# Kernel optimization log

Measured on AMD Instinct MI355X. Metric: run time of the kernel, lower is better.

## Reference

```python
import jax, jax.numpy as jnp
import numpy as np

S = 8192  # query length
T = 8192  # key/value length
D = 256   # head dim


def setup_inputs() -> dict:
    key = jax.random.key(0)
    kq, kk, kv = jax.random.split(key, 3)
    return {
        "query": jax.random.normal(kq, (S, D), dtype=jnp.float32),
        "key": jax.random.normal(kk, (T, D), dtype=jnp.float32),
        "value": jax.random.normal(kv, (T, D), dtype=jnp.float32),
    }


def reference(query, key, value):
    # attn_weights = Q @ K^T  (contract last dims, no batch dims)  -> [S, T]
    attn_weights = jnp.einsum("sd,td->st", query, key)
    # SoftmaxAttn: softmax over axes [ndim//2, ndim) == last axis for 2D
    attn_weights = jax.nn.softmax(attn_weights, axis=-1).astype(jnp.float32)
    # y = A @ V  -> [S, D]
    y = jnp.einsum("st,td->sd", attn_weights, value)
    return y
```

## Files before the change

kernel.cpp:

```cpp
#include <hip/hip_runtime.h>
#include <hip/hip_fp16.h>

#define S_LEN 8192
#define T_LEN 8192
#define D_DIM 256
#define QBLK 128
#define KVBLK 32
#define TSPLIT 8
#define TCHUNK (T_LEN / TSPLIT)
#define NKV (TCHUNK / KVBLK)
#define NQT (S_LEN / QBLK)
#define KTILE_BYTES 16384
#define VTILE_BYTES 16384
#define RESCALE_THR 6.0f
#define LOG2E 1.44269504f

typedef _Float16 f16x8 __attribute__((ext_vector_type(8)));
typedef float f32x4 __attribute__((ext_vector_type(4)));

struct h4 { _Float16 h[4]; };

#define GLOAD_LDS16(g, l)                                              \
    __builtin_amdgcn_global_load_lds(                                  \
        (const __attribute__((address_space(1))) void*)(g),            \
        (__attribute__((address_space(3))) void*)(l), 16, 0, 0)

#define MFMA16(a, b, c) __builtin_amdgcn_mfma_f32_16x16x32_f16(a, b, c, 0, 0, 0)

__global__ __launch_bounds__(256) void cvt_kernel(const float* __restrict__ in,
                                                  _Float16* __restrict__ out, int n4) {
    int i = blockIdx.x * 256 + threadIdx.x;
    if (i < n4) {
        float4 v = ((const float4*)in)[i];
        h4 o;
        o.h[0] = (_Float16)(v.x * LOG2E); o.h[1] = (_Float16)(v.y * LOG2E);
        o.h[2] = (_Float16)(v.z * LOG2E); o.h[3] = (_Float16)(v.w * LOG2E);
        ((h4*)out)[i] = o;
    }
}

__global__ __launch_bounds__(256) void cvt_swz_kernel(const float* __restrict__ in,
                                                      _Float16* __restrict__ img,
                                                      int nchunks) {
    int id = blockIdx.x * 256 + threadIdx.x;
    if (id >= nchunks) return;
    int row = id >> 5, ck = id & 31;
    int t = row >> 5, r = row & 31;
    float4 a = *(const float4*)(in + (size_t)row * D_DIM + ck * 8);
    float4 b = *(const float4*)(in + (size_t)row * D_DIM + ck * 8 + 4);
    f16x8 o;
    o[0] = (_Float16)a.x; o[1] = (_Float16)a.y; o[2] = (_Float16)a.z; o[3] = (_Float16)a.w;
    o[4] = (_Float16)b.x; o[5] = (_Float16)b.y; o[6] = (_Float16)b.z; o[7] = (_Float16)b.w;
    *(f16x8*)((char*)img + (size_t)t * KTILE_BYTES + r * 512 + ((ck ^ (r & 7)) << 4)) = o;
}

__global__ __launch_bounds__(256) void vt_swz_kernel(const float* __restrict__ V,
                                                     _Float16* __restrict__ Vimg) {
    __shared__ float tile[32][260];
    const int t = blockIdx.x;
#pragma unroll
    for (int i = 0; i < 8; ++i) {
        int idx = i * 256 + threadIdx.x;
        int kr = idx >> 6, c4 = idx & 63;
        float4 v = *(const float4*)(V + ((size_t)t * 32 + kr) * D_DIM + c4 * 4);
        tile[kr][c4 * 4 + 0] = v.x;
        tile[kr][c4 * 4 + 1] = v.y;
        tile[kr][c4 * 4 + 2] = v.z;
        tile[kr][c4 * 4 + 3] = v.w;
    }
    __syncthreads();
#pragma unroll
    for (int i = 0; i < 4; ++i) {
        int gid = i * 256 + threadIdx.x;
        int d = gid >> 2, gk = gid & 3;
        f16x8 o;
#pragma unroll
        for (int j = 0; j < 8; ++j)
            o[j] = (_Float16)tile[(j >> 2) * 16 + gk * 4 + (j & 3)][d];
        *(f16x8*)((char*)Vimg + (size_t)t * VTILE_BYTES + d * 64 +
                  ((gk ^ ((d >> 1) & 3)) << 4)) = o;
    }
}

__global__ __launch_bounds__(256, 2) void attn_kernel(
    const _Float16* __restrict__ Qh, const _Float16* __restrict__ Kimg,
    const _Float16* __restrict__ Vimg, _Float16* __restrict__ Opart,
    float* __restrict__ ml) {
    __shared__ __align__(16) char smem[65536];
    const int tid = threadIdx.x;
    const int wave = tid >> 6, lane = tid & 63;
    const int g = lane >> 4, c = lane & 15;
    const int qtile = blockIdx.x, split = blockIdx.y;
    const int tile0 = split * NKV;

    f16x8 qf[2][8];
    {
        const size_t qrow0 = (size_t)qtile * QBLK + wave * 32 + c;
#pragma unroll
        for (int mi = 0; mi < 2; ++mi)
#pragma unroll
            for (int ks = 0; ks < 8; ++ks)
                qf[mi][ks] =
                    *(const f16x8*)(Qh + (qrow0 + mi * 16) * D_DIM + (ks * 4 + g) * 8);
    }
    asm volatile("s_waitcnt vmcnt(0)" ::: "memory");

    f32x4 acc[2][16];
#pragma unroll
    for (int mi = 0; mi < 2; ++mi)
#pragma unroll
        for (int dt = 0; dt < 16; ++dt) acc[mi][dt] = (f32x4){0.f, 0.f, 0.f, 0.f};
    float m[2] = {-1e30f, -1e30f}, l[2] = {0.f, 0.f};

    const int othr = tid * 16;

    {
        const char* Kt = (const char*)Kimg + (size_t)tile0 * KTILE_BYTES;
        const char* Vt = (const char*)Vimg + (size_t)tile0 * VTILE_BYTES;
#pragma unroll
        for (int i = 0; i < 4; ++i) {
            GLOAD_LDS16(Kt + i * 4096 + othr, smem + i * 4096 + othr);
            GLOAD_LDS16(Vt + i * 4096 + othr, smem + 32768 + i * 4096 + othr);
        }
    }

    for (int kt = 0; kt < NKV; ++kt) {
        const int cur = kt & 1;
        if (kt + 1 < NKV) {
            const char* Kt = (const char*)Kimg + (size_t)(tile0 + kt + 1) * KTILE_BYTES;
            const char* Vt = (const char*)Vimg + (size_t)(tile0 + kt + 1) * VTILE_BYTES;
            const int nb = (cur ^ 1) * 16384;
#pragma unroll
            for (int i = 0; i < 4; ++i) {
                GLOAD_LDS16(Kt + i * 4096 + othr, smem + nb + i * 4096 + othr);
                GLOAD_LDS16(Vt + i * 4096 + othr, smem + 32768 + nb + i * 4096 + othr);
            }
            asm volatile("s_waitcnt vmcnt(8)" ::: "memory");
        } else {
            asm volatile("s_waitcnt vmcnt(0)" ::: "memory");
        }
        __builtin_amdgcn_s_barrier();

        const char* sK = smem + cur * 16384;
        const char* sV = smem + 32768 + cur * 16384;

        f32x4 st[2][2];
#pragma unroll
        for (int mi = 0; mi < 2; ++mi)
#pragma unroll
            for (int ct = 0; ct < 2; ++ct) st[mi][ct] = (f32x4){0.f, 0.f, 0.f, 0.f};
        __builtin_amdgcn_s_setprio(1);
#pragma unroll
        for (int ks = 0; ks < 8; ++ks) {
            const int ck = ((ks * 4 + g) ^ (c & 7)) << 4;
            f16x8 kf0 = *(const f16x8*)(sK + c * 512 + ck);
            f16x8 kf1 = *(const f16x8*)(sK + 8192 + c * 512 + ck);
            st[0][0] = MFMA16(kf0, qf[0][ks], st[0][0]);
            st[0][1] = MFMA16(kf1, qf[0][ks], st[0][1]);
            st[1][0] = MFMA16(kf0, qf[1][ks], st[1][0]);
            st[1][1] = MFMA16(kf1, qf[1][ks], st[1][1]);
        }
        __builtin_amdgcn_s_setprio(0);

        union PU { unsigned int u[4]; f16x8 v; };
        PU pu[2];
#pragma unroll
        for (int mi = 0; mi < 2; ++mi) {
            float pm = st[mi][0][0];
#pragma unroll
            for (int ct = 0; ct < 2; ++ct)
#pragma unroll
                for (int r = 0; r < 4; ++r) pm = fmaxf(pm, st[mi][ct][r]);
            pm = fmaxf(pm, __shfl_xor(pm, 16));
            pm = fmaxf(pm, __shfl_xor(pm, 32));
            if (__any(pm > m[mi] + RESCALE_THR)) {
                float mn = fmaxf(m[mi], pm);
                float sc = exp2f(m[mi] - mn);
                m[mi] = mn;
                l[mi] *= sc;
                float fr[4];
#pragma unroll
                for (int r = 0; r < 4; ++r) fr[r] = __shfl(sc, (g << 4) | (g * 4 + r));
#pragma unroll
                for (int dt = 0; dt < 16; ++dt)
#pragma unroll
                    for (int r = 0; r < 4; ++r) acc[mi][dt][r] *= fr[r];
            }
            float rs = 0.f;
#pragma unroll
            for (int ct = 0; ct < 2; ++ct)
#pragma unroll
                for (int r = 0; r < 4; ++r) {
                    float p = exp2f(st[mi][ct][r] - m[mi]);
                    st[mi][ct][r] = p;
                    rs += p;
                }
            rs += __shfl_xor(rs, 16);
            rs += __shfl_xor(rs, 32);
            l[mi] += rs;
            pu[mi].u[0] = __builtin_bit_cast(
                unsigned int, __builtin_amdgcn_cvt_pkrtz(st[mi][0][0], st[mi][0][1]));
            pu[mi].u[1] = __builtin_bit_cast(
                unsigned int, __builtin_amdgcn_cvt_pkrtz(st[mi][0][2], st[mi][0][3]));
            pu[mi].u[2] = __builtin_bit_cast(
                unsigned int, __builtin_amdgcn_cvt_pkrtz(st[mi][1][0], st[mi][1][1]));
            pu[mi].u[3] = __builtin_bit_cast(
                unsigned int, __builtin_amdgcn_cvt_pkrtz(st[mi][1][2], st[mi][1][3]));
        }

        __builtin_amdgcn_s_setprio(1);
#pragma unroll
        for (int dt = 0; dt < 16; ++dt) {
            const int d = dt * 16 + c;
            f16x8 vf = *(const f16x8*)(sV + d * 64 + ((g ^ ((c >> 1) & 3)) << 4));
            acc[0][dt] = MFMA16(pu[0].v, vf, acc[0][dt]);
            acc[1][dt] = MFMA16(pu[1].v, vf, acc[1][dt]);
        }
        __builtin_amdgcn_s_setprio(0);

        __builtin_amdgcn_s_barrier();
    }

    _Float16* Ob = Opart + (size_t)(qtile * TSPLIT + split) * QBLK * D_DIM;
#pragma unroll
    for (int mi = 0; mi < 2; ++mi)
#pragma unroll
        for (int dt = 0; dt < 16; ++dt)
#pragma unroll
            for (int r = 0; r < 4; ++r) {
                int row = wave * 32 + mi * 16 + g * 4 + r;
                int col = dt * 16 + c;
                Ob[(size_t)row * D_DIM + col] = (_Float16)acc[mi][dt][r];
            }
    if (g == 0) {
        float* mlb = ml + (size_t)((qtile * TSPLIT + split) * QBLK) * 2;
#pragma unroll
        for (int mi = 0; mi < 2; ++mi) {
            int row = wave * 32 + mi * 16 + c;
            mlb[row * 2 + 0] = m[mi];
            mlb[row * 2 + 1] = l[mi];
        }
    }
}

__global__ __launch_bounds__(256) void combine_kernel(const _Float16* __restrict__ Opart,
                                                      const float* __restrict__ ml,
                                                      float* __restrict__ out) {
    int r = blockIdx.x;
    int qtile = r >> 7, rl = r & 127;
    int d = threadIdx.x;
    float mv[TSPLIT], lv[TSPLIT];
    float M = -1e30f;
#pragma unroll
    for (int s = 0; s < TSPLIT; ++s) {
        const float* mlb = ml + (size_t)((qtile * TSPLIT + s) * QBLK + rl) * 2;
        mv[s] = mlb[0];
        lv[s] = mlb[1];
        M = fmaxf(M, mv[s]);
    }
    float num = 0.f, den = 0.f;
#pragma unroll
    for (int s = 0; s < TSPLIT; ++s) {
        float w = exp2f(mv[s] - M);
        num += w * (float)Opart[((size_t)(qtile * TSPLIT + s) * QBLK + rl) * D_DIM + d];
        den += w * lv[s];
    }
    out[(size_t)r * D_DIM + d] = num / den;
}

extern "C" void kernel_launch(void* const* d_in, const int* in_sizes, int n_in,
                              void* d_out, int out_size, void* d_ws, size_t ws_size,
                              hipStream_t stream) {
    const float* Q = (const float*)d_in[0];
    const float* K = (const float*)d_in[1];
    const float* V = (const float*)d_in[2];
    float* out = (float*)d_out;
    char* ws = (char*)d_ws;

    _Float16* Qh = (_Float16*)ws;
    _Float16* Kimg = (_Float16*)(ws + (4 << 20));
    _Float16* Vimg = (_Float16*)(ws + (8 << 20));
    _Float16* Opart = (_Float16*)(ws + (12 << 20));
    float* ml = (float*)(ws + (44 << 20));

    const int n4 = S_LEN * D_DIM / 4;
    const int nchunks = S_LEN * D_DIM / 8;
    cvt_kernel<<<n4 / 256, 256, 0, stream>>>(Q, Qh, n4);
    cvt_swz_kernel<<<nchunks / 256, 256, 0, stream>>>(K, Kimg, nchunks);
    vt_swz_kernel<<<T_LEN / 32, 256, 0, stream>>>(V, Vimg);
    dim3 ag(NQT, TSPLIT);
    attn_kernel<<<ag, 256, 0, stream>>>(Qh, Kimg, Vimg, Opart, ml);
    combine_kernel<<<S_LEN, 256, 0, stream>>>(Opart, ml, out);
}
```

Measured before the change: 110.7 us.

## Halve query block, single-buffer K/V with staggered loads and MFMA-friendly layouts

Shrinks the query block to 64 rows with 128-thread workgroups and halves shared memory, aiming at more resident workgroups. K and V are now single-buffered: V for the current tile is loaded while QK^T runs, and the next K tile is loaded while PV runs, in place of a full double buffer. K and V images are rewritten into linear per-lane layouts so LDS reads need no XOR swizzle. Row-sum reductions are deferred to the end, max shuffles happen only when a rescale fires, and exp2 uses the hardware instruction. The risks are more exposed load latency and possible LDS bank conflicts from the unswizzled layouts.

Measured after the change: 108.6 us. About the same (-1.9%).

```diff
diff --git a/kernel.cpp b/kernel.cpp
--- a/kernel.cpp
+++ b/kernel.cpp
@@ -4,11 +4,10 @@
 #define S_LEN 8192
 #define T_LEN 8192
 #define D_DIM 256
-#define QBLK 128
+#define QBLK 64
 #define KVBLK 32
 #define TSPLIT 8
-#define TCHUNK (T_LEN / TSPLIT)
-#define NKV (TCHUNK / KVBLK)
+#define NKV ((T_LEN / TSPLIT) / KVBLK)
 #define NQT (S_LEN / QBLK)
 #define KTILE_BYTES 16384
 #define VTILE_BYTES 16384
@@ -26,6 +25,16 @@
         (__attribute__((address_space(3))) void*)(l), 16, 0, 0)
 
 #define MFMA16(a, b, c) __builtin_amdgcn_mfma_f32_16x16x32_f16(a, b, c, 0, 0, 0)
+
+#if __has_builtin(__builtin_amdgcn_exp2f)
+#define EXP2(x) __builtin_amdgcn_exp2f(x)
+#else
+static __device__ __forceinline__ float EXP2(float x) {
+    float y;
+    asm("v_exp_f32 %0, %1" : "=v"(y) : "v"(x));
+    return y;
+}
+#endif
 
 __global__ __launch_bounds__(256) void cvt_kernel(const float* __restrict__ in,
                                                   _Float16* __restrict__ out, int n4) {
@@ -44,14 +53,15 @@
                                                       int nchunks) {
     int id = blockIdx.x * 256 + threadIdx.x;
     if (id >= nchunks) return;
-    int row = id >> 5, ck = id & 31;
+    int row = id >> 5, gr = id & 31;
     int t = row >> 5, r = row & 31;
-    float4 a = *(const float4*)(in + (size_t)row * D_DIM + ck * 8);
-    float4 b = *(const float4*)(in + (size_t)row * D_DIM + ck * 8 + 4);
+    float4 a = *(const float4*)(in + (size_t)row * D_DIM + gr * 8);
+    float4 b = *(const float4*)(in + (size_t)row * D_DIM + gr * 8 + 4);
     f16x8 o;
     o[0] = (_Float16)a.x; o[1] = (_Float16)a.y; o[2] = (_Float16)a.z; o[3] = (_Float16)a.w;
     o[4] = (_Float16)b.x; o[5] = (_Float16)b.y; o[6] = (_Float16)b.z; o[7] = (_Float16)b.w;
-    *(f16x8*)((char*)img + (size_t)t * KTILE_BYTES + r * 512 + ((ck ^ (r & 7)) << 4)) = o;
+    *(f16x8*)((char*)img + (size_t)t * KTILE_BYTES + (gr >> 2) * 2048 +
+              ((r >> 4) << 10) + ((r & 15) << 6) + ((gr & 3) << 4)) = o;
 }
 
 __global__ __launch_bounds__(256) void vt_swz_kernel(const float* __restrict__ V,
@@ -77,21 +87,26 @@
 #pragma unroll
         for (int j = 0; j < 8; ++j)
             o[j] = (_Float16)tile[(j >> 2) * 16 + gk * 4 + (j & 3)][d];
-        *(f16x8*)((char*)Vimg + (size_t)t * VTILE_BYTES + d * 64 +
-                  ((gk ^ ((d >> 1) & 3)) << 4)) = o;
-    }
-}
-
-__global__ __launch_bounds__(256, 2) void attn_kernel(
+        *(f16x8*)((char*)Vimg + (size_t)t * VTILE_BYTES + ((d >> 4) << 10) +
+                  (gk << 8) + ((d & 15) << 4)) = o;
+    }
+}
+
+__global__ __launch_bounds__(128, 2) void attn_kernel(
     const _Float16* __restrict__ Qh, const _Float16* __restrict__ Kimg,
     const _Float16* __restrict__ Vimg, _Float16* __restrict__ Opart,
     float* __restrict__ ml) {
-    __shared__ __align__(16) char smem[65536];
+    __shared__ __align__(16) char smem[32768];
+    char* sK = smem;
+    char* sV = smem + 16384;
     const int tid = threadIdx.x;
     const int wave = tid >> 6, lane = tid & 63;
     const int g = lane >> 4, c = lane & 15;
     const int qtile = blockIdx.x, split = blockIdx.y;
     const int tile0 = split * NKV;
+    const int othr = tid * 16;
+    const int kbase = ((lane & 15) << 6) | ((lane >> 4) << 4);
+    const int vbase = lane << 4;
 
     f16x8 qf[2][8];
     {
@@ -103,46 +118,31 @@
                 qf[mi][ks] =
                     *(const f16x8*)(Qh + (qrow0 + mi * 16) * D_DIM + (ks * 4 + g) * 8);
     }
-    asm volatile("s_waitcnt vmcnt(0)" ::: "memory");
-
-    f32x4 acc[2][16];
-#pragma unroll
-    for (int mi = 0; mi < 2; ++mi)
-#pragma unroll
-        for (int dt = 0; dt < 16; ++dt) acc[mi][dt] = (f32x4){0.f, 0.f, 0.f, 0.f};
-    float m[2] = {-1e30f, -1e30f}, l[2] = {0.f, 0.f};
-
-    const int othr = tid * 16;
 
     {
         const char* Kt = (const char*)Kimg + (size_t)tile0 * KTILE_BYTES;
-        const char* Vt = (const char*)Vimg + (size_t)tile0 * VTILE_BYTES;
-#pragma unroll
-        for (int i = 0; i < 4; ++i) {
-            GLOAD_LDS16(Kt + i * 4096 + othr, smem + i * 4096 + othr);
-            GLOAD_LDS16(Vt + i * 4096 + othr, smem + 32768 + i * 4096 + othr);
-        }
-    }
+#pragma unroll
+        for (int i = 0; i < 8; ++i) GLOAD_LDS16(Kt + i * 2048 + othr, sK + i * 2048 + othr);
+    }
+
+    f32x4 acc[2][16];
+#pragma unroll
+    for (int mi = 0; mi < 2; ++mi)
+#pragma unroll
+        for (int dt = 0; dt < 16; ++dt) acc[mi][dt] = (f32x4){0.f, 0.f, 0.f, 0.f};
+    float m[2] = {-1e30f, -1e30f};
+    float l[2] = {0.f, 0.f};
 
     for (int kt = 0; kt < NKV; ++kt) {
-        const int cur = kt & 1;
-        if (kt + 1 < NKV) {
-            const char* Kt = (const char*)Kimg + (size_t)(tile0 + kt + 1) * KTILE_BYTES;
-            const char* Vt = (const char*)Vimg + (size_t)(tile0 + kt + 1) * VTILE_BYTES;
-            const int nb = (cur ^ 1) * 16384;
-#pragma unroll
-            for (int i = 0; i < 4; ++i) {
-                GLOAD_LDS16(Kt + i * 4096 + othr, smem + nb + i * 4096 + othr);
-                GLOAD_LDS16(Vt + i * 4096 + othr, smem + 32768 + nb + i * 4096 + othr);
-            }
-            asm volatile("s_waitcnt vmcnt(8)" ::: "memory");
-        } else {
-            asm volatile("s_waitcnt vmcnt(0)" ::: "memory");
-        }
+        asm volatile("s_waitcnt vmcnt(0)" ::: "memory");
         __builtin_amdgcn_s_barrier();
 
-        const char* sK = smem + cur * 16384;
-        const char* sV = smem + 32768 + cur * 16384;
+        {
+            const char* Vt = (const char*)Vimg + (size_t)(tile0 + kt) * VTILE_BYTES;
+#pragma unroll
+            for (int i = 0; i < 8; ++i)
+                GLOAD_LDS16(Vt + i * 2048 + othr, sV + i * 2048 + othr);
+        }
 
         f32x4 st[2][2];
 #pragma unroll
@@ -152,9 +152,8 @@
         __builtin_amdgcn_s_setprio(1);
 #pragma unroll
         for (int ks = 0; ks < 8; ++ks) {
-            const int ck = ((ks * 4 + g) ^ (c & 7)) << 4;
-            f16x8 kf0 = *(const f16x8*)(sK + c * 512 + ck);
-            f16x8 kf1 = *(const f16x8*)(sK + 8192 + c * 512 + ck);
+            f16x8 kf0 = *(const f16x8*)(sK + ks * 2048 + kbase);
+            f16x8 kf1 = *(const f16x8*)(sK + ks * 2048 + 1024 + kbase);
             st[0][0] = MFMA16(kf0, qf[0][ks], st[0][0]);
             st[0][1] = MFMA16(kf1, qf[0][ks], st[0][1]);
             st[1][0] = MFMA16(kf0, qf[1][ks], st[1][0]);
@@ -166,16 +165,15 @@
         PU pu[2];
 #pragma unroll
         for (int mi = 0; mi < 2; ++mi) {
-            float pm = st[mi][0][0];
-#pragma unroll
-            for (int ct = 0; ct < 2; ++ct)
-#pragma unroll
-                for (int r = 0; r < 4; ++r) pm = fmaxf(pm, st[mi][ct][r]);
-            pm = fmaxf(pm, __shfl_xor(pm, 16));
-            pm = fmaxf(pm, __shfl_xor(pm, 32));
+            float pm = fmaxf(fmaxf(fmaxf(st[mi][0][0], st[mi][0][1]),
+                                   fmaxf(st[mi][0][2], st[mi][0][3])),
+                             fmaxf(fmaxf(st[mi][1][0], st[mi][1][1]),
+                                   fmaxf(st[mi][1][2], st[mi][1][3])));
             if (__any(pm > m[mi] + RESCALE_THR)) {
+                pm = fmaxf(pm, __shfl_xor(pm, 16));
+                pm = fmaxf(pm, __shfl_xor(pm, 32));
                 float mn = fmaxf(m[mi], pm);
-                float sc = exp2f(m[mi] - mn);
+                float sc = EXP2(m[mi] - mn);
                 m[mi] = mn;
                 l[mi] *= sc;
                 float fr[4];
@@ -191,12 +189,10 @@
             for (int ct = 0; ct < 2; ++ct)
 #pragma unroll
                 for (int r = 0; r < 4; ++r) {
-                    float p = exp2f(st[mi][ct][r] - m[mi]);
+                    float p = EXP2(st[mi][ct][r] - m[mi]);
                     st[mi][ct][r] = p;
                     rs += p;
                 }
-            rs += __shfl_xor(rs, 16);
-            rs += __shfl_xor(rs, 32);
             l[mi] += rs;
             pu[mi].u[0] = __builtin_bit_cast(
                 unsigned int, __builtin_amdgcn_cvt_pkrtz(st[mi][0][0], st[mi][0][1]));
@@ -208,17 +204,24 @@
                 unsigned int, __builtin_amdgcn_cvt_pkrtz(st[mi][1][2], st[mi][1][3]));
         }
 
+        asm volatile("s_waitcnt vmcnt(0)" ::: "memory");
+        __builtin_amdgcn_s_barrier();
+
+        if (kt + 1 < NKV) {
+            const char* Kt = (const char*)Kimg + (size_t)(tile0 + kt + 1) * KTILE_BYTES;
+#pragma unroll
+            for (int i = 0; i < 8; ++i)
+                GLOAD_LDS16(Kt + i * 2048 + othr, sK + i * 2048 + othr);
+        }
+
         __builtin_amdgcn_s_setprio(1);
 #pragma unroll
         for (int dt = 0; dt < 16; ++dt) {
-            const int d = dt * 16 + c;
-            f16x8 vf = *(const f16x8*)(sV + d * 64 + ((g ^ ((c >> 1) & 3)) << 4));
+            f16x8 vf = *(const f16x8*)(sV + dt * 1024 + vbase);
             acc[0][dt] = MFMA16(pu[0].v, vf, acc[0][dt]);
             acc[1][dt] = MFMA16(pu[1].v, vf, acc[1][dt]);
         }
         __builtin_amdgcn_s_setprio(0);
-
-        __builtin_amdgcn_s_barrier();
     }
 
     _Float16* Ob = Opart + (size_t)(qtile * TSPLIT + split) * QBLK * D_DIM;
@@ -232,6 +235,11 @@
                 int col = dt * 16 + c;
                 Ob[(size_t)row * D_DIM + col] = (_Float16)acc[mi][dt][r];
             }
+#pragma unroll
+    for (int mi = 0; mi < 2; ++mi) {
+        l[mi] += __shfl_xor(l[mi], 16);
+        l[mi] += __shfl_xor(l[mi], 32);
+    }
     if (g == 0) {
         float* mlb = ml + (size_t)((qtile * TSPLIT + split) * QBLK) * 2;
 #pragma unroll
@@ -247,7 +255,7 @@
                                                       const float* __restrict__ ml,
                                                       float* __restrict__ out) {
     int r = blockIdx.x;
-    int qtile = r >> 7, rl = r & 127;
+    int qtile = r >> 6, rl = r & 63;
     int d = threadIdx.x;
     float mv[TSPLIT], lv[TSPLIT];
     float M = -1e30f;
@@ -261,7 +269,7 @@
     float num = 0.f, den = 0.f;
 #pragma unroll
     for (int s = 0; s < TSPLIT; ++s) {
-        float w = exp2f(mv[s] - M);
+        float w = EXP2(mv[s] - M);
         num += w * (float)Opart[((size_t)(qtile * TSPLIT + s) * QBLK + rl) * D_DIM + d];
         den += w * lv[s];
     }
@@ -281,14 +289,15 @@
     _Float16* Kimg = (_Float16*)(ws + (4 << 20));
     _Float16* Vimg = (_Float16*)(ws + (8 << 20));
     _Float16* Opart = (_Float16*)(ws + (12 << 20));
-    float* ml = (float*)(ws + (44 << 20));
+    float* ml = (float*)(ws + ((size_t)44 << 20));
 
     const int n4 = S_LEN * D_DIM / 4;
     const int nchunks = S_LEN * D_DIM / 8;
     cvt_kernel<<<n4 / 256, 256, 0, stream>>>(Q, Qh, n4);
     cvt_swz_kernel<<<nchunks / 256, 256, 0, stream>>>(K, Kimg, nchunks);
     vt_swz_kernel<<<T_LEN / 32, 256, 0, stream>>>(V, Vimg);
+
     dim3 ag(NQT, TSPLIT);
-    attn_kernel<<<ag, 256, 0, stream>>>(Qh, Kimg, Vimg, Opart, ml);
+    attn_kernel<<<ag, 128, 0, stream>>>(Qh, Kimg, Vimg, Opart, ml);
     combine_kernel<<<S_LEN, 256, 0, stream>>>(Opart, ml, out);
 }
```
